# Kernel tuning notes

Measured on AMD Instinct MI355X. Metric: run time of the kernel, lower is better.

The kernel has to match this reference:

```python
import jax, jax.numpy as jnp
import numpy as np

D_MODEL = 1024
NUM_HEADS = 16
D_K = D_MODEL // NUM_HEADS
B, S = 4, 2048
NEG = -1e10


def setup_inputs() -> dict:
    key = jax.random.key(0)
    ks = jax.random.split(key, 12)
    sc = 1.0 / np.sqrt(D_MODEL)
    inp = {
        "q": jax.random.normal(ks[0], (B, S, D_MODEL), jnp.float32),
        "k": jax.random.normal(ks[1], (B, S, D_MODEL), jnp.float32),
        "v": jax.random.normal(ks[2], (B, S, D_MODEL), jnp.float32),
        "mask": jnp.broadcast_to(jnp.tril(jnp.ones((S, S), jnp.int32)), (B, 1, S, S)),
        "w_q": jax.random.normal(ks[3], (D_MODEL, D_MODEL), jnp.float32) * sc,
        "b_q": jax.random.normal(ks[4], (D_MODEL,), jnp.float32) * 0.02,
        "w_k": jax.random.normal(ks[5], (D_MODEL, D_MODEL), jnp.float32) * sc,
        "b_k": jax.random.normal(ks[6], (D_MODEL,), jnp.float32) * 0.02,
        "w_v": jax.random.normal(ks[7], (D_MODEL, D_MODEL), jnp.float32) * sc,
        "b_v": jax.random.normal(ks[8], (D_MODEL,), jnp.float32) * 0.02,
        "w_o": jax.random.normal(ks[9], (D_MODEL, D_MODEL), jnp.float32) * sc,
        "b_o": jax.random.normal(ks[10], (D_MODEL,), jnp.float32) * 0.02,
    }
    return inp


def reference(q, k, v, mask, w_q, b_q, w_k, b_k, w_v, b_v, w_o, b_o):
    b = q.shape[0]
    split = lambda x: x.reshape(b, -1, NUM_HEADS, D_K).transpose(0, 2, 1, 3)  # [B,H,S,d_k]
    Q = split(q @ w_q.T + b_q)
    K = split(k @ w_k.T + b_k)
    V = split(v @ w_v.T + b_v)
    energy = jnp.einsum("bhqd,bhkd->bhqk", Q, K) / jnp.sqrt(jnp.float32(D_K))
    energy = jnp.where(mask == 0, jnp.float32(NEG), energy)
    attn = jax.nn.softmax(energy, axis=-1)
    out = jnp.einsum("bhqk,bhkd->bhqd", attn, V)
    out = out.transpose(0, 2, 1, 3).reshape(b, -1, D_MODEL)
    return out @ w_o.T + b_o
```

## Files before the change

kernel.cpp:

```cpp
#include <hip/hip_runtime.h>

typedef unsigned short u16;
typedef unsigned int u32;
typedef short short8 __attribute__((ext_vector_type(8)));
typedef u16 u16x8 __attribute__((ext_vector_type(8)));
typedef u16 u16x4 __attribute__((ext_vector_type(4)));
typedef float f32x4 __attribute__((ext_vector_type(4)));
typedef float f32x16 __attribute__((ext_vector_type(16)));

__device__ __forceinline__ u16 f2bf(float f) {
  u32 u = __builtin_bit_cast(u32, f);
  u += 0x7fff + ((u >> 16) & 1);
  return (u16)(u >> 16);
}
__device__ __forceinline__ float ex2(float x) {
  float r; asm("v_exp_f32 %0, %1" : "=v"(r) : "v"(x)); return r;
}
__device__ __forceinline__ u32 cvtpk(float lo, float hi) {
  u32 r; asm("v_cvt_pk_bf16_f32 %0, %1, %2" : "=v"(r) : "v"(lo), "v"(hi)); return r;
}

__device__ __forceinline__ void gload16(const u16* g, u16* l) {
  __builtin_amdgcn_global_load_lds(
      (const __attribute__((address_space(1))) u32*)(unsigned long long)(const void*)g,
      (__attribute__((address_space(3))) u32*)(u32)(unsigned long long)(void*)l,
      16, 0, 0);
}

#define NB 8192
#define WB 1024

__global__ __launch_bounds__(256) void cvt_all(
    const float* __restrict__ q, const float* __restrict__ k, const float* __restrict__ v,
    const float* __restrict__ wq, const float* __restrict__ wk, const float* __restrict__ wv,
    const float* __restrict__ wo, u16* __restrict__ Xq, u16* __restrict__ Xk,
    u16* __restrict__ Xv, u16* __restrict__ Wq, u16* __restrict__ Wk, u16* __restrict__ Wv,
    u16* __restrict__ Wo) {
  int bid = blockIdx.x;
  const float* s; u16* d; int x;
  if (bid < 3 * NB) {
    int z = bid / NB; x = bid - z * NB;
    s = z == 0 ? q : (z == 1 ? k : v);
    d = z == 0 ? Xq : (z == 1 ? Xk : Xv);
  } else {
    int r = bid - 3 * NB;
    int z = r / WB; x = r - z * WB;
    s = z == 0 ? wq : (z == 1 ? wk : (z == 2 ? wv : wo));
    d = z == 0 ? Wq : (z == 1 ? Wk : (z == 2 ? Wv : Wo));
  }
  int i = x * 256 + threadIdx.x;
  float4 f = reinterpret_cast<const float4*>(s)[i];
  u16x4 o;
  o.x = f2bf(f.x); o.y = f2bf(f.y); o.z = f2bf(f.z); o.w = f2bf(f.w);
  reinterpret_cast<u16x4*>(d)[i] = o;
}

template <int BM>
__device__ __forceinline__ void gemm_core(const u16* __restrict__ A, const u16* __restrict__ Bm,
                                          const float* __restrict__ bias, u16* __restrict__ Cb,
                                          float* __restrict__ Cf, int K, int ldc, int ccol0,
                                          float cs) {
  constexpr int MI = BM / 32;
  __shared__ __align__(16) u16 As[3][BM * 32];
  __shared__ __align__(16) u16 Bs[3][128 * 32];
  const int t = threadIdx.x, l = t & 63, w = t >> 6;
  const int lg = l >> 4, lr = l & 15;
  const int m0 = blockIdx.y * BM, n0 = blockIdx.x * 128;
  const int wr = (w >> 1) * (16 * MI), wc = (w & 1) * 64;
  const int srowA = (BM == 128) ? (w * 32 + (l >> 2)) : (w * 16 + (l >> 2));
  const int srowB = w * 32 + (l >> 2);
  const int scol = ((l & 3) ^ ((l >> 3) & 3)) * 8;
  const u16* ga = A + (size_t)(m0 + srowA) * K + scol;
  const u16* gb = Bm + (size_t)(n0 + srowB) * K + scol;
  const int ldstA = (BM == 128) ? (w * 1024 + l * 8) : (w * 512 + l * 8);
  const int ldstB = w * 1024 + l * 8;
  const int ko = (lg ^ ((lr >> 1) & 3)) * 8;

  u16* a0 = &As[0][0]; u16* a1 = &As[1][0]; u16* a2 = &As[2][0];
  u16* b0 = &Bs[0][0]; u16* b1 = &Bs[1][0]; u16* b2 = &Bs[2][0];

  auto stage = [&](int kk, u16* ab, u16* bb) {
    gload16(ga + kk, ab + ldstA);
    if constexpr (BM == 128) gload16(ga + kk + 16 * (size_t)K, ab + ldstA + 512);
    gload16(gb + kk, bb + ldstB);
    gload16(gb + kk + 16 * (size_t)K, bb + ldstB + 512);
  };
  auto wait_counted = [&]() {
    if constexpr (BM == 128) asm volatile("s_waitcnt vmcnt(4)" ::: "memory");
    else                     asm volatile("s_waitcnt vmcnt(3)" ::: "memory");
  };

  f32x4 acc[MI][4];
#pragma unroll
  for (int i = 0; i < MI; ++i)
#pragma unroll
    for (int jj = 0; jj < 4; ++jj) acc[i][jj] = (f32x4){0.f, 0.f, 0.f, 0.f};

  const int ni = K >> 5;
  stage(0, a0, b0);
  stage(32, a1, b1);
  wait_counted();
  __builtin_amdgcn_s_barrier();
  __builtin_amdgcn_sched_barrier(0);

  for (int it = 0; it < ni; ++it) {
    const bool pf = (it + 2) < ni;
    if (pf) stage((it + 2) << 5, a2, b2);
    short8 af[MI], bf[4];
#pragma unroll
    for (int i = 0; i < MI; ++i)
      af[i] = *reinterpret_cast<const short8*>(&a0[(wr + 16 * i + lr) * 32 + ko]);
#pragma unroll
    for (int jj = 0; jj < 4; ++jj)
      bf[jj] = *reinterpret_cast<const short8*>(&b0[(wc + 16 * jj + lr) * 32 + ko]);
    __builtin_amdgcn_s_setprio(1);
#pragma unroll
    for (int i = 0; i < MI; ++i)
#pragma unroll
      for (int jj = 0; jj < 4; ++jj)
        acc[i][jj] = __builtin_amdgcn_mfma_f32_16x16x32_bf16(af[i], bf[jj], acc[i][jj], 0, 0, 0);
    __builtin_amdgcn_s_setprio(0);
    if (it + 1 < ni) {
      if (pf) wait_counted();
      else    asm volatile("s_waitcnt vmcnt(0)" ::: "memory");
      __builtin_amdgcn_s_barrier();
      __builtin_amdgcn_sched_barrier(0);
    }
    u16* tmp;
    tmp = a0; a0 = a1; a1 = a2; a2 = tmp;
    tmp = b0; b0 = b1; b1 = b2; b2 = tmp;
  }

#pragma unroll
  for (int i = 0; i < MI; ++i) {
#pragma unroll
    for (int jj = 0; jj < 4; ++jj) {
      int col = n0 + wc + 16 * jj + lr;
      float bv = bias[col];
#pragma unroll
      for (int r = 0; r < 4; ++r) {
        int row = m0 + wr + 16 * i + lg * 4 + r;
        float val = (acc[i][jj][r] + bv) * cs;
        if (Cb) Cb[(size_t)row * ldc + ccol0 + col] = f2bf(val);
        else    Cf[(size_t)row * ldc + col] = val;
      }
    }
  }
}

#define QSCALE 0.18033688011112042f

__global__ __launch_bounds__(256) void gemm_qkv(const u16* __restrict__ Xq, const u16* __restrict__ Xk,
                                                const u16* __restrict__ Xv, const u16* __restrict__ Wq,
                                                const u16* __restrict__ Wk, const u16* __restrict__ Wv,
                                                const float* __restrict__ bq, const float* __restrict__ bk,
                                                const float* __restrict__ bv, u16* __restrict__ QKV) {
  const int z = blockIdx.z;
  const u16* A = z == 0 ? Xq : (z == 1 ? Xk : Xv);
  const u16* B = z == 0 ? Wq : (z == 1 ? Wk : Wv);
  const float* bias = z == 0 ? bq : (z == 1 ? bk : bv);
  gemm_core<128>(A, B, bias, QKV, nullptr, 1024, 3072, z * 1024, z == 0 ? QSCALE : 1.0f);
}

__global__ __launch_bounds__(256) void gemm_out(const u16* __restrict__ AO, const u16* __restrict__ Wo,
                                                const float* __restrict__ bo, float* __restrict__ out) {
  gemm_core<64>(AO, Wo, bo, nullptr, out, 1024, 1024, 0, 1.0f);
}

#define LDK 72
#define DEFER_THR 11.0f

__global__ __launch_bounds__(256, 3) void attn_fwd(const u16* __restrict__ QKV, u16* __restrict__ O) {
  __shared__ __align__(16) u16 Kt[2][64 * LDK];
  __shared__ __align__(16) u16 Vt[2][64 * LDK];

  const int t = threadIdx.x, l = t & 63, w = t >> 6;
  const int lq = l & 31, hi = l >> 5;
  const int bh = blockIdx.x;
  const int qb = 15 - (int)blockIdx.y;
  const int b = bh >> 4, h = bh & 15;
  const size_t rowb = (size_t)b * 2048;
  const int qcol = h * 64, kcol = 1024 + h * 64, vcol = 2048 + h * 64;
  const int q0w = qb * 128 + 32 * w;
  const int nt = 2 * qb + 2;

  short8 qf[4];
  {
    const u16* qp = QKV + (rowb + q0w + lq) * 3072 + qcol + hi * 8;
#pragma unroll
    for (int ks = 0; ks < 4; ++ks) qf[ks] = *reinterpret_cast<const short8*>(qp + ks * 16);
  }

  f32x16 oa[2];
#pragma unroll
  for (int dt = 0; dt < 2; ++dt)
#pragma unroll
    for (int r = 0; r < 16; ++r) oa[dt][r] = 0.f;
  float m_run = -1e30f, l_run = 0.f;

  const int kr = t & 31, kc = (t >> 5) * 8;
  short8 ka0, ka1;
  u16x8 va0, va1;

  auto stage_load = [&](int kv64) {
    const u16* kp = QKV + (rowb + (size_t)kv64 * 64 + kr) * 3072 + kcol + kc;
    ka0 = *reinterpret_cast<const short8*>(kp);
    ka1 = *reinterpret_cast<const short8*>(kp + 32 * 3072);
    const u16* vp = QKV + (rowb + (size_t)kv64 * 64 + 2 * kr) * 3072 + vcol + kc;
    va0 = *reinterpret_cast<const u16x8*>(vp);
    va1 = *reinterpret_cast<const u16x8*>(vp + 3072);
  };
  auto stage_write = [&](int buf) {
    *reinterpret_cast<short8*>(&Kt[buf][kr * LDK + kc]) = ka0;
    *reinterpret_cast<short8*>(&Kt[buf][(kr + 32) * LDK + kc]) = ka1;
#pragma unroll
    for (int jj = 0; jj < 8; ++jj) {
      u32 pk = (u32)va0[jj] | ((u32)va1[jj] << 16);
      *reinterpret_cast<u32*>(&Vt[buf][(kc + jj) * LDK + 2 * kr]) = pk;
    }
  };

  auto packP = [&](const f32x16& p, short8 pf[2]) {
    u32 P[8], X[8];
#pragma unroll
    for (int m2 = 0; m2 < 8; ++m2) {
      P[m2] = cvtpk(p[2 * m2], p[2 * m2 + 1]);
      X[m2] = (u32)__shfl_xor((int)P[m2], 32);
    }
#pragma unroll
    for (int ks2 = 0; ks2 < 2; ++ks2) {
      union { u32 u[4]; short8 v; } uu;
      uu.u[0] = hi ? X[4 * ks2 + 2] : P[4 * ks2 + 0];
      uu.u[1] = hi ? X[4 * ks2 + 3] : P[4 * ks2 + 1];
      uu.u[2] = hi ? P[4 * ks2 + 2] : X[4 * ks2 + 0];
      uu.u[3] = hi ? P[4 * ks2 + 3] : X[4 * ks2 + 1];
      pf[ks2] = uu.v;
    }
  };
  auto pvStep = [&](const u16* Vtc, int kt32, const short8 pf[2]) {
    __builtin_amdgcn_s_setprio(1);
#pragma unroll
    for (int ks2 = 0; ks2 < 2; ++ks2)
#pragma unroll
      for (int dt = 0; dt < 2; ++dt) {
        short8 vf = *reinterpret_cast<const short8*>(
            &Vtc[(dt * 32 + lq) * LDK + kt32 + ks2 * 16 + hi * 8]);
        oa[dt] = __builtin_amdgcn_mfma_f32_32x32x16_bf16(vf, pf[ks2], oa[dt], 0, 0, 0);
      }
    __builtin_amdgcn_s_setprio(0);
  };
  auto rescale_sum = [&](float pm) {
    if (!__all(pm <= m_run + DEFER_THR)) {
      float mnew = fmaxf(m_run, pm);
      float al = ex2(m_run - mnew);
      l_run *= al;
#pragma unroll
      for (int dt = 0; dt < 2; ++dt)
#pragma unroll
        for (int r = 0; r < 16; ++r) oa[dt][r] *= al;
      m_run = mnew;
    }
  };

  auto flash2 = [&](const u16* Ktc, const u16* Vtc, bool diag1) {
    f32x16 s0, s1;
#pragma unroll
    for (int r = 0; r < 16; ++r) { s0[r] = 0.f; s1[r] = 0.f; }
    __builtin_amdgcn_s_setprio(1);
#pragma unroll
    for (int ks = 0; ks < 4; ++ks) {
      short8 kf = *reinterpret_cast<const short8*>(&Ktc[lq * LDK + ks * 16 + hi * 8]);
      s0 = __builtin_amdgcn_mfma_f32_32x32x16_bf16(kf, qf[ks], s0, 0, 0, 0);
    }
#pragma unroll
    for (int ks = 0; ks < 4; ++ks) {
      short8 kf = *reinterpret_cast<const short8*>(&Ktc[(32 + lq) * LDK + ks * 16 + hi * 8]);
      s1 = __builtin_amdgcn_mfma_f32_32x32x16_bf16(kf, qf[ks], s1, 0, 0, 0);
    }
    __builtin_amdgcn_s_setprio(0);
    if (diag1) {
#pragma unroll
      for (int r = 0; r < 16; ++r) {
        int off = (r & 3) + 8 * (r >> 2) + 4 * hi;
        if (off > lq) s1[r] = -1e30f;
      }
    }
    float pm = fmaxf(s0[0], s1[0]);
#pragma unroll
    for (int r = 1; r < 16; ++r) pm = fmaxf(pm, fmaxf(s0[r], s1[r]));
    pm = fmaxf(pm, __shfl_xor(pm, 32));
    rescale_sum(pm);
    float ps = 0.f;
#pragma unroll
    for (int r = 0; r < 16; ++r) { float e = ex2(s0[r] - m_run); s0[r] = e; ps += e; }
#pragma unroll
    for (int r = 0; r < 16; ++r) { float e = ex2(s1[r] - m_run); s1[r] = e; ps += e; }
    ps += __shfl_xor(ps, 32);
    l_run += ps;
    short8 pf[2];
    packP(s0, pf);
    pvStep(Vtc, 0, pf);
    packP(s1, pf);
    pvStep(Vtc, 32, pf);
  };

  auto flash1 = [&](const u16* Ktc, const u16* Vtc) {
    f32x16 s;
#pragma unroll
    for (int r = 0; r < 16; ++r) s[r] = 0.f;
    __builtin_amdgcn_s_setprio(1);
#pragma unroll
    for (int ks = 0; ks < 4; ++ks) {
      short8 kf = *reinterpret_cast<const short8*>(&Ktc[lq * LDK + ks * 16 + hi * 8]);
      s = __builtin_amdgcn_mfma_f32_32x32x16_bf16(kf, qf[ks], s, 0, 0, 0);
    }
    __builtin_amdgcn_s_setprio(0);
#pragma unroll
    for (int r = 0; r < 16; ++r) {
      int off = (r & 3) + 8 * (r >> 2) + 4 * hi;
      if (off > lq) s[r] = -1e30f;
    }
    float pm = s[0];
#pragma unroll
    for (int r = 1; r < 16; ++r) pm = fmaxf(pm, s[r]);
    pm = fmaxf(pm, __shfl_xor(pm, 32));
    rescale_sum(pm);
    float ps = 0.f;
#pragma unroll
    for (int r = 0; r < 16; ++r) { float e = ex2(s[r] - m_run); s[r] = e; ps += e; }
    ps += __shfl_xor(ps, 32);
    l_run += ps;
    short8 pf[2];
    packP(s, pf);
    pvStep(Vtc, 0, pf);
  };

  stage_load(0);
  stage_write(0);
  __syncthreads();

  for (int kb = 0; kb < nt; ++kb) {
    const int cur = kb & 1;
    const u16* Ktc = &Kt[cur][0];
    const u16* Vtc = &Vt[cur][0];
    if (kb + 1 < nt) stage_load(kb + 1);
    const int rel = q0w - kb * 64;
    if (rel >= 32)      flash2(Ktc, Vtc, rel == 32);
    else if (rel == 0)  flash1(Ktc, Vtc);
    if (kb + 1 < nt) stage_write(cur ^ 1);
    __syncthreads();
  }

  const float inv = __builtin_amdgcn_rcpf(l_run);
  const size_t obase = (rowb + q0w + lq) * 1024 + h * 64;
#pragma unroll
  for (int dt = 0; dt < 2; ++dt) {
    u32 Bp[8], Xb[8];
#pragma unroll
    for (int m2 = 0; m2 < 8; ++m2) {
      Bp[m2] = cvtpk(oa[dt][2 * m2] * inv, oa[dt][2 * m2 + 1] * inv);
      Xb[m2] = (u32)__shfl_xor((int)Bp[m2], 32);
    }
    if (hi == dt) {
#pragma unroll
      for (int c = 0; c < 4; ++c) {
        union { u32 u[4]; short8 v; } uu;
        uu.u[0] = hi ? Xb[2 * c]     : Bp[2 * c];
        uu.u[1] = hi ? Xb[2 * c + 1] : Bp[2 * c + 1];
        uu.u[2] = hi ? Bp[2 * c]     : Xb[2 * c];
        uu.u[3] = hi ? Bp[2 * c + 1] : Xb[2 * c + 1];
        *reinterpret_cast<short8*>(&O[obase + dt * 32 + c * 8]) = uu.v;
      }
    }
  }
}

extern "C" void kernel_launch(void* const* d_in, const int* in_sizes, int n_in,
                              void* d_out, int out_size, void* d_ws, size_t ws_size,
                              hipStream_t stream) {
  const float* q  = (const float*)d_in[0];
  const float* k  = (const float*)d_in[1];
  const float* v  = (const float*)d_in[2];
  const float* wq = (const float*)d_in[4];
  const float* bq = (const float*)d_in[5];
  const float* wk = (const float*)d_in[6];
  const float* bk = (const float*)d_in[7];
  const float* wv = (const float*)d_in[8];
  const float* bv = (const float*)d_in[9];
  const float* wo = (const float*)d_in[10];
  const float* bo = (const float*)d_in[11];
  float* out = (float*)d_out;

  u16* ws = (u16*)d_ws;
  const size_t NE = 8192ull * 1024;
  const size_t WE = 1024ull * 1024;
  u16* Xq   = ws;
  u16* Xk   = Xq + NE;
  u16* Xv   = Xk + NE;
  u16* Wq   = Xv + NE;
  u16* Wk   = Wq + WE;
  u16* Wv   = Wk + WE;
  u16* Wo   = Wv + WE;
  u16* QKVp = Wo + WE;
  u16* AO   = QKVp + 8192ull * 3072;

  cvt_all<<<3 * NB + 4 * WB, 256, 0, stream>>>(q, k, v, wq, wk, wv, wo,
                                               Xq, Xk, Xv, Wq, Wk, Wv, Wo);

  gemm_qkv<<<dim3(8, 64, 3), 256, 0, stream>>>(Xq, Xk, Xv, Wq, Wk, Wv, bq, bk, bv, QKVp);

  attn_fwd<<<dim3(64, 16), 256, 0, stream>>>(QKVp, AO);

  gemm_out<<<dim3(8, 128), 256, 0, stream>>>(AO, Wo, bo, out);
}
```

Before: 356.9 us.

## Fuse fp32-to-bf16 activation conversion into QKV GEMM and remap block order

Drops the separate conversion pass over the q/k/v activations. The QKV GEMM now streams fp32 activation tiles straight into LDS through an XOR-swizzled layout and packs them to bf16 in registers before the MFMA. Both GEMMs also remap block IDs so that blocks launched together are spread across rows and column tiles, which is meant to improve L2 reuse. The trade-off is twice the A-tile LDS footprint and global traffic for fp32 in the GEMM, plus extra conversion instructions in its inner loop, in exchange for skipping a full write and re-read of the bf16 activations.

```diff
diff --git a/kernel.cpp b/kernel.cpp
--- a/kernel.cpp
+++ b/kernel.cpp
@@ -20,74 +20,71 @@
   u32 r; asm("v_cvt_pk_bf16_f32 %0, %1, %2" : "=v"(r) : "v"(lo), "v"(hi)); return r;
 }
 
-__device__ __forceinline__ void gload16(const u16* g, u16* l) {
+__device__ __forceinline__ void gload16(const void* g, void* l) {
   __builtin_amdgcn_global_load_lds(
-      (const __attribute__((address_space(1))) u32*)(unsigned long long)(const void*)g,
-      (__attribute__((address_space(3))) u32*)(u32)(unsigned long long)(void*)l,
+      (const __attribute__((address_space(1))) u32*)(unsigned long long)g,
+      (__attribute__((address_space(3))) u32*)(u32)(unsigned long long)l,
       16, 0, 0);
 }
 
-#define NB 8192
-#define WB 1024
-
-__global__ __launch_bounds__(256) void cvt_all(
-    const float* __restrict__ q, const float* __restrict__ k, const float* __restrict__ v,
-    const float* __restrict__ wq, const float* __restrict__ wk, const float* __restrict__ wv,
-    const float* __restrict__ wo, u16* __restrict__ Xq, u16* __restrict__ Xk,
-    u16* __restrict__ Xv, u16* __restrict__ Wq, u16* __restrict__ Wk, u16* __restrict__ Wv,
-    u16* __restrict__ Wo) {
-  int bid = blockIdx.x;
-  const float* s; u16* d; int x;
-  if (bid < 3 * NB) {
-    int z = bid / NB; x = bid - z * NB;
-    s = z == 0 ? q : (z == 1 ? k : v);
-    d = z == 0 ? Xq : (z == 1 ? Xk : Xv);
-  } else {
-    int r = bid - 3 * NB;
-    int z = r / WB; x = r - z * WB;
-    s = z == 0 ? wq : (z == 1 ? wk : (z == 2 ? wv : wo));
-    d = z == 0 ? Wq : (z == 1 ? Wk : (z == 2 ? Wv : Wo));
-  }
-  int i = x * 256 + threadIdx.x;
+__global__ __launch_bounds__(256) void cvt4(const float* __restrict__ a, const float* __restrict__ b,
+                                            const float* __restrict__ c, const float* __restrict__ d0,
+                                            u16* __restrict__ oa, u16* __restrict__ ob,
+                                            u16* __restrict__ oc, u16* __restrict__ od, int n4) {
+  const int z = blockIdx.y;
+  const float* s = z == 0 ? a : (z == 1 ? b : (z == 2 ? c : d0));
+  u16* d = z == 0 ? oa : (z == 1 ? ob : (z == 2 ? oc : od));
+  int i = blockIdx.x * 256 + threadIdx.x;
+  if (i >= n4) return;
   float4 f = reinterpret_cast<const float4*>(s)[i];
   u16x4 o;
   o.x = f2bf(f.x); o.y = f2bf(f.y); o.z = f2bf(f.z); o.w = f2bf(f.w);
   reinterpret_cast<u16x4*>(d)[i] = o;
 }
 
-template <int BM>
-__device__ __forceinline__ void gemm_core(const u16* __restrict__ A, const u16* __restrict__ Bm,
+template <int BM, bool AF32>
+__device__ __forceinline__ void gemm_core(const void* __restrict__ Ap, const u16* __restrict__ Bm,
                                           const float* __restrict__ bias, u16* __restrict__ Cb,
                                           float* __restrict__ Cf, int K, int ldc, int ccol0,
-                                          float cs) {
+                                          float cs, int m0, int n0) {
   constexpr int MI = BM / 32;
-  __shared__ __align__(16) u16 As[3][BM * 32];
+  __shared__ __align__(16) u16 As[3][AF32 ? BM * 64 : BM * 32];
   __shared__ __align__(16) u16 Bs[3][128 * 32];
   const int t = threadIdx.x, l = t & 63, w = t >> 6;
   const int lg = l >> 4, lr = l & 15;
-  const int m0 = blockIdx.y * BM, n0 = blockIdx.x * 128;
   const int wr = (w >> 1) * (16 * MI), wc = (w & 1) * 64;
-  const int srowA = (BM == 128) ? (w * 32 + (l >> 2)) : (w * 16 + (l >> 2));
   const int srowB = w * 32 + (l >> 2);
   const int scol = ((l & 3) ^ ((l >> 3) & 3)) * 8;
-  const u16* ga = A + (size_t)(m0 + srowA) * K + scol;
   const u16* gb = Bm + (size_t)(n0 + srowB) * K + scol;
-  const int ldstA = (BM == 128) ? (w * 1024 + l * 8) : (w * 512 + l * 8);
   const int ldstB = w * 1024 + l * 8;
   const int ko = (lg ^ ((lr >> 1) & 3)) * 8;
 
+  const int srowA = w * 16 + (l >> 2);
+  const u16* ga = (const u16*)Ap + (size_t)(m0 + srowA) * K + scol;
+  const int ldstA = w * 512 + l * 8;
+  const float* gaf = (const float*)Ap +
+      (size_t)(m0 + w * 32 + (l >> 3)) * K + (((l & 7) ^ (l >> 3)) * 4);
+
   u16* a0 = &As[0][0]; u16* a1 = &As[1][0]; u16* a2 = &As[2][0];
   u16* b0 = &Bs[0][0]; u16* b1 = &Bs[1][0]; u16* b2 = &Bs[2][0];
 
   auto stage = [&](int kk, u16* ab, u16* bb) {
-    gload16(ga + kk, ab + ldstA);
-    if constexpr (BM == 128) gload16(ga + kk + 16 * (size_t)K, ab + ldstA + 512);
     gload16(gb + kk, bb + ldstB);
     gload16(gb + kk + 16 * (size_t)K, bb + ldstB + 512);
+    if constexpr (AF32) {
+#pragma unroll
+      for (int c = 0; c < 4; ++c)
+        gload16(gaf + kk + (size_t)(c * 8) * K,
+                (float*)ab + (w * 32 + c * 8) * 32 + l * 4);
+    } else {
+      gload16(ga + kk, ab + ldstA);
+      if constexpr (BM == 128) gload16(ga + kk + 16 * (size_t)K, ab + ldstA + 512);
+    }
   };
   auto wait_counted = [&]() {
-    if constexpr (BM == 128) asm volatile("s_waitcnt vmcnt(4)" ::: "memory");
-    else                     asm volatile("s_waitcnt vmcnt(3)" ::: "memory");
+    if constexpr (AF32)            asm volatile("s_waitcnt vmcnt(6)" ::: "memory");
+    else if constexpr (BM == 128)  asm volatile("s_waitcnt vmcnt(4)" ::: "memory");
+    else                           asm volatile("s_waitcnt vmcnt(3)" ::: "memory");
   };
 
   f32x4 acc[MI][4];
@@ -108,8 +105,21 @@
     if (pf) stage((it + 2) << 5, a2, b2);
     short8 af[MI], bf[4];
 #pragma unroll
-    for (int i = 0; i < MI; ++i)
-      af[i] = *reinterpret_cast<const short8*>(&a0[(wr + 16 * i + lr) * 32 + ko]);
+    for (int i = 0; i < MI; ++i) {
+      if constexpr (AF32) {
+        const float* abuf = (const float*)a0;
+        const int arow = wr + 16 * i + lr;
+        const int s7 = arow & 7;
+        f32x4 u = *reinterpret_cast<const f32x4*>(abuf + arow * 32 + ((2 * lg) ^ s7) * 4);
+        f32x4 v = *reinterpret_cast<const f32x4*>(abuf + arow * 32 + ((2 * lg + 1) ^ s7) * 4);
+        union { u32 x[4]; short8 s; } pk;
+        pk.x[0] = cvtpk(u[0], u[1]); pk.x[1] = cvtpk(u[2], u[3]);
+        pk.x[2] = cvtpk(v[0], v[1]); pk.x[3] = cvtpk(v[2], v[3]);
+        af[i] = pk.s;
+      } else {
+        af[i] = *reinterpret_cast<const short8*>(&a0[(wr + 16 * i + lr) * 32 + ko]);
+      }
+    }
 #pragma unroll
     for (int jj = 0; jj < 4; ++jj)
       bf[jj] = *reinterpret_cast<const short8*>(&b0[(wc + 16 * jj + lr) * 32 + ko]);
@@ -150,21 +160,30 @@
 
 #define QSCALE 0.18033688011112042f
 
-__global__ __launch_bounds__(256) void gemm_qkv(const u16* __restrict__ Xq, const u16* __restrict__ Xk,
-                                                const u16* __restrict__ Xv, const u16* __restrict__ Wq,
+__global__ __launch_bounds__(256) void gemm_qkv(const float* __restrict__ q, const float* __restrict__ k,
+                                                const float* __restrict__ v, const u16* __restrict__ Wq,
                                                 const u16* __restrict__ Wk, const u16* __restrict__ Wv,
                                                 const float* __restrict__ bq, const float* __restrict__ bk,
                                                 const float* __restrict__ bv, u16* __restrict__ QKV) {
-  const int z = blockIdx.z;
-  const u16* A = z == 0 ? Xq : (z == 1 ? Xk : Xv);
+  const int hw = blockIdx.x + 8 * (blockIdx.y + 64 * blockIdx.z);
+  const int lgid = (hw & 7) * 192 + (hw >> 3);
+  const int n0 = (lgid & 7) * 128;
+  const int m0 = ((lgid >> 3) & 63) * 128;
+  const int z = lgid >> 9;
+  const float* A = z == 0 ? q : (z == 1 ? k : v);
   const u16* B = z == 0 ? Wq : (z == 1 ? Wk : Wv);
   const float* bias = z == 0 ? bq : (z == 1 ? bk : bv);
-  gemm_core<128>(A, B, bias, QKV, nullptr, 1024, 3072, z * 1024, z == 0 ? QSCALE : 1.0f);
+  gemm_core<128, true>(A, B, bias, QKV, nullptr, 1024, 3072, z * 1024,
+                       z == 0 ? QSCALE : 1.0f, m0, n0);
 }
 
 __global__ __launch_bounds__(256) void gemm_out(const u16* __restrict__ AO, const u16* __restrict__ Wo,
                                                 const float* __restrict__ bo, float* __restrict__ out) {
-  gemm_core<64>(AO, Wo, bo, nullptr, out, 1024, 1024, 0, 1.0f);
+  const int hw = blockIdx.x + 8 * blockIdx.y;
+  const int lgid = (hw & 7) * 128 + (hw >> 3);
+  const int n0 = (lgid & 7) * 128;
+  const int m0 = (lgid >> 3) * 64;
+  gemm_core<64, false>(AO, Wo, bo, nullptr, out, 1024, 1024, 0, 1.0f, m0, n0);
 }
 
 #define LDK 72
@@ -392,22 +411,17 @@
   float* out = (float*)d_out;
 
   u16* ws = (u16*)d_ws;
-  const size_t NE = 8192ull * 1024;
   const size_t WE = 1024ull * 1024;
-  u16* Xq   = ws;
-  u16* Xk   = Xq + NE;
-  u16* Xv   = Xk + NE;
-  u16* Wq   = Xv + NE;
+  u16* Wq   = ws;
   u16* Wk   = Wq + WE;
   u16* Wv   = Wk + WE;
   u16* Wo   = Wv + WE;
   u16* QKVp = Wo + WE;
   u16* AO   = QKVp + 8192ull * 3072;
 
-  cvt_all<<<3 * NB + 4 * WB, 256, 0, stream>>>(q, k, v, wq, wk, wv, wo,
-                                               Xq, Xk, Xv, Wq, Wk, Wv, Wo);
-
-  gemm_qkv<<<dim3(8, 64, 3), 256, 0, stream>>>(Xq, Xk, Xv, Wq, Wk, Wv, bq, bk, bv, QKVp);
+  cvt4<<<dim3(1024, 4), 256, 0, stream>>>(wq, wk, wv, wo, Wq, Wk, Wv, Wo, (int)(WE / 4));
+
+  gemm_qkv<<<dim3(8, 64, 3), 256, 0, stream>>>(q, k, v, Wq, Wk, Wv, bq, bk, bv, QKVp);
 
   attn_fwd<<<dim3(64, 16), 256, 0, stream>>>(QKVp, AO);
 
```

After: 392.4 us. 1.1x slower.
